# Optimization experiments

Hardware: AMD Instinct MI355X
Metric: run time of the kernel (lower is better)

Reference implementation:

```python
import jax, jax.numpy as jnp
import numpy as np

N_NODES = 50000
N_EDGES = 1600000
D = 128
N_CLASSES = 21


def setup_inputs() -> dict:
    key = jax.random.key(0)
    k1, k2, k3, k4, k5 = jax.random.split(key, 5)
    s = 1.0 / np.sqrt(D)
    return {
        "node_embedding": jax.random.normal(k1, (N_NODES, D), dtype=jnp.float32),
        "edge_index": jax.random.randint(k2, (2, N_EDGES), 0, N_NODES, dtype=jnp.int64),
        "W_fuse_src": jax.random.normal(k3, (D, D), dtype=jnp.float32) * s,
        "W_fuse_dst": jax.random.normal(k4, (D, D), dtype=jnp.float32) * s,
        "b_fuse": jnp.zeros((D,), dtype=jnp.float32),
        "W_cls": jax.random.normal(k5, (D, N_CLASSES), dtype=jnp.float32) * s,
        "b_cls": jnp.zeros((N_CLASSES,), dtype=jnp.float32),
    }


def reference(node_embedding, edge_index, W_fuse_src, W_fuse_dst, b_fuse, W_cls, b_cls):
    # Batched version of the per-edge Python loop:
    # gather src/dst node embeddings for every edge, fuse, classify.
    src = node_embedding[edge_index[0]]  # [E, D]
    dst = node_embedding[edge_index[1]]  # [E, D]
    # node_fusion: concat(src, dst) @ W -> split into two [D, D] blocks
    fused = src @ W_fuse_src + dst @ W_fuse_dst + b_fuse  # [E, D]
    logits = fused @ W_cls + b_cls  # [E, n_classes]
    return logits
```

## Files before the change

kernel.cpp:

```cpp
#include <hip/hip_runtime.h>
#include <hip/hip_bf16.h>

#define D 128
#define N_NODES 50000
#define N_EDGES 1600000
#define NCLS 21

typedef float vfloat4 __attribute__((ext_vector_type(4)));

#define A_OFF    0
#define BT_OFF   (128*48*4)
#define PSRC_OFF 32768
#define PDST_OFF (PSRC_OFF + N_NODES*32*2)

__global__ void ec_k1_fold(const float* __restrict__ Wsrc, const float* __restrict__ Wdst,
                           const float* __restrict__ Wcls, const float* __restrict__ bfuse,
                           const float* __restrict__ bcls, float* __restrict__ A,
                           float* __restrict__ bt) {
    int t = blockIdx.x * 256 + threadIdx.x;
    if (t < 128 * 48) {
        int k = t / 48, c48 = t % 48;
        int half = c48 / 24, c = c48 % 24;
        float v = 0.f;
        if (c < NCLS) {
            const float* W = half ? Wdst : Wsrc;
            const float* wrow = W + k * D;
#pragma unroll 4
            for (int j = 0; j < D; ++j) v += wrow[j] * Wcls[j * NCLS + c];
        }
        A[k * 48 + c48] = v;
    } else if (t < 128 * 48 + 24) {
        int c = t - 128 * 48;
        float v = 0.f;
        if (c < NCLS) {
            for (int j = 0; j < D; ++j) v += bfuse[j] * Wcls[j * NCLS + c];
            v += bcls[c];
        }
        bt[c] = v;
    }
}

__global__ __launch_bounds__(256) void ec_k2_proj(const float* __restrict__ emb,
                                                  const float* __restrict__ A,
                                                  const float* __restrict__ bt,
                                                  __hip_bfloat16* __restrict__ Psrc,
                                                  __hip_bfloat16* __restrict__ Pdst) {
    __shared__ __align__(16) float As[128 * 48];
    __shared__ __align__(16) float et[32 * 130];
    const int t = threadIdx.x;
    const int base = blockIdx.x * 128;

#pragma unroll
    for (int i = 0; i < 6; ++i) {
        int s4 = t + i * 256;
        ((float4*)As)[s4] = ((const float4*)A)[s4];
    }

    const int slot = t & 63;
    const int qb = __builtin_amdgcn_readfirstlane(t >> 6);
    const float4* Aq4 = ((const float4*)As) + qb * 3;

    float acc0[12], acc1[12];
#pragma unroll
    for (int j = 0; j < 12; ++j) { acc0[j] = 0.f; acc1[j] = 0.f; }
    if (qb < 2) {
#pragma unroll
        for (int j = 0; j < 12; ++j) {
            float b = bt[qb * 12 + j];
            acc0[j] = b; acc1[j] = b;
        }
    }

    for (int kt = 0; kt < 4; ++kt) {
        __syncthreads();
#pragma unroll
        for (int i = 0; i < 4; ++i) {
            int lin = t + i * 256;
            int n = lin >> 3, q = lin & 7;
            int gn = base + n;
            float4 v = make_float4(0.f, 0.f, 0.f, 0.f);
            if (gn < N_NODES) v = ((const float4*)(emb + (size_t)gn * D + kt * 32))[q];
            int k0 = q * 4;
            et[(k0 + 0) * 130 + n] = v.x;
            et[(k0 + 1) * 130 + n] = v.y;
            et[(k0 + 2) * 130 + n] = v.z;
            et[(k0 + 3) * 130 + n] = v.w;
        }
        __syncthreads();

#pragma unroll
        for (int kk = 0; kk < 32; ++kk) {
            int k = kt * 32 + kk;
            float e0 = et[kk * 130 + slot];
            float e1 = et[kk * 130 + slot + 64];
            float4 a0 = Aq4[k * 12 + 0];
            float4 a1 = Aq4[k * 12 + 1];
            float4 a2 = Aq4[k * 12 + 2];
            acc0[0]  += e0 * a0.x;  acc1[0]  += e1 * a0.x;
            acc0[1]  += e0 * a0.y;  acc1[1]  += e1 * a0.y;
            acc0[2]  += e0 * a0.z;  acc1[2]  += e1 * a0.z;
            acc0[3]  += e0 * a0.w;  acc1[3]  += e1 * a0.w;
            acc0[4]  += e0 * a1.x;  acc1[4]  += e1 * a1.x;
            acc0[5]  += e0 * a1.y;  acc1[5]  += e1 * a1.y;
            acc0[6]  += e0 * a1.z;  acc1[6]  += e1 * a1.z;
            acc0[7]  += e0 * a1.w;  acc1[7]  += e1 * a1.w;
            acc0[8]  += e0 * a2.x;  acc1[8]  += e1 * a2.x;
            acc0[9]  += e0 * a2.y;  acc1[9]  += e1 * a2.y;
            acc0[10] += e0 * a2.z;  acc1[10] += e1 * a2.z;
            acc0[11] += e0 * a2.w;  acc1[11] += e1 * a2.w;
        }
    }

    __hip_bfloat16* Pq = (qb < 2) ? Psrc : Pdst;
    const int coff = (qb & 1) * 12;
    int n0 = base + slot, n1 = base + slot + 64;
    if (n0 < N_NODES) {
        __hip_bfloat162* p = (__hip_bfloat162*)(Pq + (size_t)n0 * 32 + coff);
#pragma unroll
        for (int j = 0; j < 6; ++j) {
            __hip_bfloat162 h;
            h.x = __float2bfloat16(acc0[2 * j]);
            h.y = __float2bfloat16(acc0[2 * j + 1]);
            p[j] = h;
        }
    }
    if (n1 < N_NODES) {
        __hip_bfloat162* p = (__hip_bfloat162*)(Pq + (size_t)n1 * 32 + coff);
#pragma unroll
        for (int j = 0; j < 6; ++j) {
            __hip_bfloat162 h;
            h.x = __float2bfloat16(acc1[2 * j]);
            h.y = __float2bfloat16(acc1[2 * j + 1]);
            p[j] = h;
        }
    }
}

#define EPB 512
__device__ __forceinline__ float bf_lo(unsigned u) { return __uint_as_float(u << 16); }
__device__ __forceinline__ float bf_hi(unsigned u) { return __uint_as_float(u & 0xFFFF0000u); }

__global__ __launch_bounds__(256) void ec_k3_edges(const int* __restrict__ ei,
                                                   const __hip_bfloat16* __restrict__ Psrc,
                                                   const __hip_bfloat16* __restrict__ Pdst,
                                                   float* __restrict__ out) {
    __shared__ __align__(16) float sm[EPB * NCLS];
    const int t = threadIdx.x;
    const int e0 = blockIdx.x * EPB;

    int s[2], d[2];
#pragma unroll
    for (int j = 0; j < 2; ++j) {
        int e = e0 + t + j * 256;
        s[j] = __builtin_nontemporal_load(ei + e);
        d[j] = __builtin_nontemporal_load(ei + N_EDGES + e);
    }

#pragma unroll
    for (int j = 0; j < 2; ++j) {
        const uint4* ps = (const uint4*)(Psrc + (size_t)s[j] * 32);
        const uint4* pd = (const uint4*)(Pdst + (size_t)d[j] * 32);
        uint4 a0 = ps[0], a1 = ps[1];
        uint4 b0 = pd[0], b1 = pd[1];
        unsigned a2 = ((const unsigned*)(ps + 2))[0];
        unsigned a3 = ((const unsigned*)(ps + 2))[1];
        unsigned a4 = ((const unsigned*)(ps + 2))[2];
        unsigned b2 = ((const unsigned*)(pd + 2))[0];
        unsigned b3 = ((const unsigned*)(pd + 2))[1];
        unsigned b4 = ((const unsigned*)(pd + 2))[2];

        float v[NCLS];
        v[0]  = bf_lo(a0.x) + bf_lo(b0.x);  v[1]  = bf_hi(a0.x) + bf_hi(b0.x);
        v[2]  = bf_lo(a0.y) + bf_lo(b0.y);  v[3]  = bf_hi(a0.y) + bf_hi(b0.y);
        v[4]  = bf_lo(a0.z) + bf_lo(b0.z);  v[5]  = bf_hi(a0.z) + bf_hi(b0.z);
        v[6]  = bf_lo(a0.w) + bf_lo(b0.w);  v[7]  = bf_hi(a0.w) + bf_hi(b0.w);
        v[8]  = bf_lo(a1.x) + bf_lo(b1.x);  v[9]  = bf_hi(a1.x) + bf_hi(b1.x);
        v[10] = bf_lo(a1.y) + bf_lo(b1.y);  v[11] = bf_hi(a1.y) + bf_hi(b1.y);
        v[12] = bf_lo(a1.z) + bf_lo(b1.z);  v[13] = bf_hi(a1.z) + bf_hi(b1.z);
        v[14] = bf_lo(a1.w) + bf_lo(b1.w);  v[15] = bf_hi(a1.w) + bf_hi(b1.w);
        v[16] = bf_lo(a2)   + bf_lo(b2);    v[17] = bf_hi(a2)   + bf_hi(b2);
        v[18] = bf_lo(a3)   + bf_lo(b3);    v[19] = bf_hi(a3)   + bf_hi(b3);
        v[20] = bf_lo(a4)   + bf_lo(b4);

        int el = t + j * 256;
        float* row = sm + el * NCLS;
#pragma unroll
        for (int c = 0; c < NCLS; ++c) row[c] = v[c];
    }
    __syncthreads();

    const vfloat4* sm4 = (const vfloat4*)sm;
    vfloat4* o4 = (vfloat4*)(out + (size_t)e0 * NCLS);
    for (int i = t; i < EPB * NCLS / 4; i += 256)
        __builtin_nontemporal_store(sm4[i], o4 + i);
}

extern "C" void kernel_launch(void* const* d_in, const int* in_sizes, int n_in,
                              void* d_out, int out_size, void* d_ws, size_t ws_size,
                              hipStream_t stream) {
    const float* emb   = (const float*)d_in[0];
    const int*   ei    = (const int*)d_in[1];
    const float* Wsrc  = (const float*)d_in[2];
    const float* Wdst  = (const float*)d_in[3];
    const float* bfuse = (const float*)d_in[4];
    const float* Wcls  = (const float*)d_in[5];
    const float* bcls  = (const float*)d_in[6];
    float* out = (float*)d_out;

    char* ws = (char*)d_ws;
    float* A  = (float*)(ws + A_OFF);
    float* bt = (float*)(ws + BT_OFF);
    __hip_bfloat16* Psrc = (__hip_bfloat16*)(ws + PSRC_OFF);
    __hip_bfloat16* Pdst = (__hip_bfloat16*)(ws + PDST_OFF);

    ec_k1_fold<<<(128 * 48 + 24 + 255) / 256, 256, 0, stream>>>(Wsrc, Wdst, Wcls, bfuse, bcls, A, bt);
    ec_k2_proj<<<(N_NODES + 127) / 128, 256, 0, stream>>>(emb, A, bt, Psrc, Pdst);
    ec_k3_edges<<<N_EDGES / EPB, 256, 0, stream>>>(ei, Psrc, Pdst, out);
}
```

Before: 227.3 us.

## Make edge kernel one thread per output element and prefetch node tiles

The edge kernel now uses one thread per (edge, class) output element. Each thread reads its own edge indices and gathers a single bf16 value from each projection table, then stores straight to the output. This drops the large shared-memory staging buffer, which limited occupancy, in exchange for repeated index loads and scalar 2-byte gathers. The projection kernel also register-prefetches the next embedding k-tile while the current one is written to LDS, and reads two adjacent nodes per thread with a float2 LDS load, which changes which nodes each thread owns.

Result: slower. 265.6 us (+16.8%).

```diff
diff --git a/kernel.cpp b/kernel.cpp
--- a/kernel.cpp
+++ b/kernel.cpp
@@ -5,8 +5,6 @@
 #define N_NODES 50000
 #define N_EDGES 1600000
 #define NCLS 21
-
-typedef float vfloat4 __attribute__((ext_vector_type(4)));
 
 #define A_OFF    0
 #define BT_OFF   (128*48*4)
@@ -60,6 +58,17 @@
     const int qb = __builtin_amdgcn_readfirstlane(t >> 6);
     const float4* Aq4 = ((const float4*)As) + qb * 3;
 
+    const int pn = t >> 3;
+    const int pq = t & 7;
+
+    float4 pf[4];
+#pragma unroll
+    for (int i = 0; i < 4; ++i) {
+        int gn = base + pn + i * 32;
+        pf[i] = make_float4(0.f, 0.f, 0.f, 0.f);
+        if (gn < N_NODES) pf[i] = ((const float4*)(emb + (size_t)gn * D))[pq];
+    }
+
     float acc0[12], acc1[12];
 #pragma unroll
     for (int j = 0; j < 12; ++j) { acc0[j] = 0.f; acc1[j] = 0.f; }
@@ -75,24 +84,29 @@
         __syncthreads();
 #pragma unroll
         for (int i = 0; i < 4; ++i) {
-            int lin = t + i * 256;
-            int n = lin >> 3, q = lin & 7;
-            int gn = base + n;
-            float4 v = make_float4(0.f, 0.f, 0.f, 0.f);
-            if (gn < N_NODES) v = ((const float4*)(emb + (size_t)gn * D + kt * 32))[q];
-            int k0 = q * 4;
-            et[(k0 + 0) * 130 + n] = v.x;
-            et[(k0 + 1) * 130 + n] = v.y;
-            et[(k0 + 2) * 130 + n] = v.z;
-            et[(k0 + 3) * 130 + n] = v.w;
+            int n = pn + i * 32;
+            int k0 = pq * 4;
+            et[(k0 + 0) * 130 + n] = pf[i].x;
+            et[(k0 + 1) * 130 + n] = pf[i].y;
+            et[(k0 + 2) * 130 + n] = pf[i].z;
+            et[(k0 + 3) * 130 + n] = pf[i].w;
+        }
+        if (kt < 3) {
+#pragma unroll
+            for (int i = 0; i < 4; ++i) {
+                int gn = base + pn + i * 32;
+                float4 v = make_float4(0.f, 0.f, 0.f, 0.f);
+                if (gn < N_NODES) v = ((const float4*)(emb + (size_t)gn * D + (kt + 1) * 32))[pq];
+                pf[i] = v;
+            }
         }
         __syncthreads();
 
 #pragma unroll
         for (int kk = 0; kk < 32; ++kk) {
             int k = kt * 32 + kk;
-            float e0 = et[kk * 130 + slot];
-            float e1 = et[kk * 130 + slot + 64];
+            float2 e01 = *(const float2*)&et[kk * 130 + 2 * slot];
+            float e0 = e01.x, e1 = e01.y;
             float4 a0 = Aq4[k * 12 + 0];
             float4 a1 = Aq4[k * 12 + 1];
             float4 a2 = Aq4[k * 12 + 2];
@@ -113,7 +127,7 @@
 
     __hip_bfloat16* Pq = (qb < 2) ? Psrc : Pdst;
     const int coff = (qb & 1) * 12;
-    int n0 = base + slot, n1 = base + slot + 64;
+    int n0 = base + 2 * slot, n1 = n0 + 1;
     if (n0 < N_NODES) {
         __hip_bfloat162* p = (__hip_bfloat162*)(Pq + (size_t)n0 * 32 + coff);
 #pragma unroll
@@ -136,63 +150,19 @@
     }
 }
 
-#define EPB 512
-__device__ __forceinline__ float bf_lo(unsigned u) { return __uint_as_float(u << 16); }
-__device__ __forceinline__ float bf_hi(unsigned u) { return __uint_as_float(u & 0xFFFF0000u); }
-
 __global__ __launch_bounds__(256) void ec_k3_edges(const int* __restrict__ ei,
                                                    const __hip_bfloat16* __restrict__ Psrc,
                                                    const __hip_bfloat16* __restrict__ Pdst,
                                                    float* __restrict__ out) {
-    __shared__ __align__(16) float sm[EPB * NCLS];
-    const int t = threadIdx.x;
-    const int e0 = blockIdx.x * EPB;
-
-    int s[2], d[2];
-#pragma unroll
-    for (int j = 0; j < 2; ++j) {
-        int e = e0 + t + j * 256;
-        s[j] = __builtin_nontemporal_load(ei + e);
-        d[j] = __builtin_nontemporal_load(ei + N_EDGES + e);
-    }
-
-#pragma unroll
-    for (int j = 0; j < 2; ++j) {
-        const uint4* ps = (const uint4*)(Psrc + (size_t)s[j] * 32);
-        const uint4* pd = (const uint4*)(Pdst + (size_t)d[j] * 32);
-        uint4 a0 = ps[0], a1 = ps[1];
-        uint4 b0 = pd[0], b1 = pd[1];
-        unsigned a2 = ((const unsigned*)(ps + 2))[0];
-        unsigned a3 = ((const unsigned*)(ps + 2))[1];
-        unsigned a4 = ((const unsigned*)(ps + 2))[2];
-        unsigned b2 = ((const unsigned*)(pd + 2))[0];
-        unsigned b3 = ((const unsigned*)(pd + 2))[1];
-        unsigned b4 = ((const unsigned*)(pd + 2))[2];
-
-        float v[NCLS];
-        v[0]  = bf_lo(a0.x) + bf_lo(b0.x);  v[1]  = bf_hi(a0.x) + bf_hi(b0.x);
-        v[2]  = bf_lo(a0.y) + bf_lo(b0.y);  v[3]  = bf_hi(a0.y) + bf_hi(b0.y);
-        v[4]  = bf_lo(a0.z) + bf_lo(b0.z);  v[5]  = bf_hi(a0.z) + bf_hi(b0.z);
-        v[6]  = bf_lo(a0.w) + bf_lo(b0.w);  v[7]  = bf_hi(a0.w) + bf_hi(b0.w);
-        v[8]  = bf_lo(a1.x) + bf_lo(b1.x);  v[9]  = bf_hi(a1.x) + bf_hi(b1.x);
-        v[10] = bf_lo(a1.y) + bf_lo(b1.y);  v[11] = bf_hi(a1.y) + bf_hi(b1.y);
-        v[12] = bf_lo(a1.z) + bf_lo(b1.z);  v[13] = bf_hi(a1.z) + bf_hi(b1.z);
-        v[14] = bf_lo(a1.w) + bf_lo(b1.w);  v[15] = bf_hi(a1.w) + bf_hi(b1.w);
-        v[16] = bf_lo(a2)   + bf_lo(b2);    v[17] = bf_hi(a2)   + bf_hi(b2);
-        v[18] = bf_lo(a3)   + bf_lo(b3);    v[19] = bf_hi(a3)   + bf_hi(b3);
-        v[20] = bf_lo(a4)   + bf_lo(b4);
-
-        int el = t + j * 256;
-        float* row = sm + el * NCLS;
-#pragma unroll
-        for (int c = 0; c < NCLS; ++c) row[c] = v[c];
-    }
-    __syncthreads();
-
-    const vfloat4* sm4 = (const vfloat4*)sm;
-    vfloat4* o4 = (vfloat4*)(out + (size_t)e0 * NCLS);
-    for (int i = t; i < EPB * NCLS / 4; i += 256)
-        __builtin_nontemporal_store(sm4[i], o4 + i);
+    int idx = blockIdx.x * 256 + threadIdx.x;
+    if (idx >= N_EDGES * NCLS) return;
+    int e = idx / NCLS;
+    int c = idx - e * NCLS;
+    int s = ei[e];
+    int d = ei[N_EDGES + e];
+    float v = __bfloat162float(Psrc[(size_t)s * 32 + c]) +
+              __bfloat162float(Pdst[(size_t)d * 32 + c]);
+    __builtin_nontemporal_store(v, out + idx);
 }
 
 extern "C" void kernel_launch(void* const* d_in, const int* in_sizes, int n_in,
@@ -215,5 +185,6 @@
 
     ec_k1_fold<<<(128 * 48 + 24 + 255) / 256, 256, 0, stream>>>(Wsrc, Wdst, Wcls, bfuse, bcls, A, bt);
     ec_k2_proj<<<(N_NODES + 127) / 128, 256, 0, stream>>>(emb, A, bt, Psrc, Pdst);
-    ec_k3_edges<<<N_EDGES / EPB, 256, 0, stream>>>(ei, Psrc, Pdst, out);
+    int total = N_EDGES * NCLS;
+    ec_k3_edges<<<(total + 255) / 256, 256, 0, stream>>>(ei, Psrc, Pdst, out);
 }
```
